# Performance work log

Measured on AMD Instinct MI355X. Metric: run time of the kernel, lower is better.

Reference implementation:

```python
import jax, jax.numpy as jnp
import numpy as np

N_NODES = 100000
N_EDGES = 1600000
IN_F = 64
HID = 64
NUM_GRAPHS = 256


def _lin(x, W, b):
    # Linear: x [N, in] @ W [in, out] + b [out]
    return x @ W + b


def _spect_conv(x, src, dst, W, b):
    # SpectConv, K=1, selfconn=False, edge_attr == 1:
    # h[i] = sum_{(j->i) in E} x[j];  out = h @ W + b
    h = jax.ops.segment_sum(x[src], dst, num_segments=N_NODES)
    return h @ W + b


def setup_inputs() -> dict:
    key = jax.random.key(0)
    ks = jax.random.split(key, 40)
    inp = {
        "x": jax.random.normal(ks[0], (N_NODES, IN_F), dtype=jnp.float32),
        "edge_index": jax.random.randint(ks[1], (2, N_EDGES), 0, N_NODES, dtype=jnp.int64),
        "batch": jnp.sort(jax.random.randint(ks[2], (N_NODES,), 0, NUM_GRAPHS, dtype=jnp.int64)),
    }
    i = 3
    def mk(shape):
        nonlocal i
        w = jax.random.normal(ks[i], shape, dtype=jnp.float32) * 0.05
        i += 1
        return w
    for l, fin in ((1, IN_F), (2, HID), (3, HID)):
        inp[f"conv{l}_w"] = mk((fin, HID)); inp[f"conv{l}_b"] = mk((HID,))
        for j in (1, 2, 3):
            inp[f"fc{l}{j}_w"] = mk((fin, HID)); inp[f"fc{l}{j}_b"] = mk((HID,))
    inp["fc1_w"] = mk((HID, 10)); inp["fc1_b"] = mk((10,))
    inp["fc2_w"] = mk((10, 1)); inp["fc2_b"] = mk((1,))
    return inp


def reference(x, edge_index, batch,
              conv1_w, conv1_b, fc11_w, fc11_b, fc12_w, fc12_b, fc13_w, fc13_b,
              conv2_w, conv2_b, fc21_w, fc21_b, fc22_w, fc22_b, fc23_w, fc23_b,
              conv3_w, conv3_b, fc31_w, fc31_b, fc32_w, fc32_b, fc33_w, fc33_b,
              fc1_w, fc1_b, fc2_w, fc2_b):
    src, dst = edge_index[0], edge_index[1]

    def layer(h, fa_w, fa_b, cw, cb, fb_w, fb_b, fc_w, fc_b):
        return jax.nn.relu(_lin(h, fa_w, fa_b)
                           + _spect_conv(h, src, dst, cw, cb)
                           + _lin(h, fb_w, fb_b) * _lin(h, fc_w, fc_b))

    h = layer(x, fc11_w, fc11_b, conv1_w, conv1_b, fc12_w, fc12_b, fc13_w, fc13_b)
    h = layer(h, fc21_w, fc21_b, conv2_w, conv2_b, fc22_w, fc22_b, fc23_w, fc23_b)
    h = layer(h, fc31_w, fc31_b, conv3_w, conv3_b, fc32_w, fc32_b, fc33_w, fc33_b)

    # global_mean_pool over graph ids
    sums = jax.ops.segment_sum(h, batch, num_segments=NUM_GRAPHS)
    cnts = jax.ops.segment_sum(jnp.ones((h.shape[0], 1), h.dtype), batch, num_segments=NUM_GRAPHS)
    pooled = sums / jnp.maximum(cnts, 1.0)

    g = _lin(pooled, fc1_w, fc1_b)
    return _lin(g, fc2_w, fc2_b)  # [NUM_GRAPHS, 1]
```

## Files before the change

kernel.cpp:

```cpp
#include <hip/hip_runtime.h>
#include <hip/hip_fp16.h>

#define NN 100000
#define NE 1600000
#define NG 256
#define NPB 32
#define LAYER_GRID 2048
#define SIDX 1280

#define BSH 9
#define NBKT ((NN + 511) / 512)
#define CAP 9216
#define TILE_A 4096
#define NBLK_A ((NE + TILE_A - 1) / TILE_A)

typedef _Float16 f16x8 __attribute__((ext_vector_type(8)));
typedef float f32x4 __attribute__((ext_vector_type(4)));

__device__ __forceinline__ uint2 f4_to_h16(float4 o) {
    __half2 lo = __floats2half2_rn(o.x, o.y);
    __half2 hi = __floats2half2_rn(o.z, o.w);
    uint2 u;
    u.x = *(unsigned int*)&lo;
    u.y = *(unsigned int*)&hi;
    return u;
}

__global__ __launch_bounds__(256) void cvt_kernel(const float* __restrict__ in,
                                                  __half* __restrict__ out) {
    const int i = blockIdx.x * 256 + threadIdx.x;
    const int n4 = NN * 64 / 4;
    if (i < n4) {
        float4 v = ((const float4*)in)[i];
        ((uint2*)out)[i] = f4_to_h16(v);
    }
}

__global__ __launch_bounds__(256) void wprep_kernel(const float* __restrict__ Wa,
                                                    const float* __restrict__ Wc,
                                                    const float* __restrict__ Wb,
                                                    const float* __restrict__ Wd,
                                                    __half* __restrict__ out) {
    const int i = blockIdx.x * 256 + threadIdx.x;
    if (i < 16384) {
        const int m = i >> 12;
        const int e = i & 4095;
        const int n = e >> 6, k = e & 63;
        const float* W = (m == 0) ? Wa : (m == 1) ? Wc : (m == 2) ? Wb : Wd;
        out[m * 4096 + n * 64 + k] = __float2half(W[k * 64 + n]);
    }
}

__global__ __launch_bounds__(256) void initcur_kernel(int* __restrict__ gcur) {
    int t = threadIdx.x;
    if (t < NBKT) gcur[t] = t * CAP;
}

__global__ __launch_bounds__(256) void binA_kernel(const int* __restrict__ src,
                                                   const int* __restrict__ dst,
                                                   int* __restrict__ gcur,
                                                   unsigned int* __restrict__ binned)
{
    __shared__ int hist[NBKT];
    __shared__ int cnt2[NBKT];
    __shared__ int lexcl[NBKT];
    __shared__ int base[NBKT];
    __shared__ int s[256];
    __shared__ unsigned int buf[TILE_A];
    __shared__ unsigned char bkt8[TILE_A];

    const int t = threadIdx.x;
    const int e0 = blockIdx.x * TILE_A;
    const int nedge = min(TILE_A, NE - e0);

    if (t < NBKT) { hist[t] = 0; cnt2[t] = 0; }
    __syncthreads();

    for (int j = t; j < nedge; j += 256)
        atomicAdd(&hist[dst[e0 + j] >> BSH], 1);
    __syncthreads();

    s[t] = (t < NBKT) ? hist[t] : 0;
    __syncthreads();
    for (int off = 1; off < 256; off <<= 1) {
        int u = (t >= off) ? s[t - off] : 0;
        __syncthreads();
        s[t] += u;
        __syncthreads();
    }
    if (t < NBKT) {
        lexcl[t] = s[t] - hist[t];
        if (hist[t] > 0) base[t] = atomicAdd(&gcur[t], hist[t]);
    }
    __syncthreads();

    for (int j = t; j < nedge; j += 256) {
        const int d = dst[e0 + j];
        const int sv = src[e0 + j];
        const int b = d >> BSH;
        const int r = atomicAdd(&cnt2[b], 1);
        const int idx = lexcl[b] + r;
        buf[idx] = ((unsigned int)sv << BSH) | (unsigned int)(d & 511);
        bkt8[idx] = (unsigned char)b;
    }
    __syncthreads();

    for (int j = t; j < nedge; j += 256) {
        const int b = bkt8[j];
        binned[base[b] + (j - lexcl[b])] = buf[j];
    }
}

__global__ __launch_bounds__(256) void bscan_kernel(const int* __restrict__ gcur,
                                                    int* __restrict__ bbase,
                                                    int* __restrict__ rs)
{
    __shared__ int s[256];
    const int t = threadIdx.x;
    const int sz = (t < NBKT) ? (gcur[t] - t * CAP) : 0;
    s[t] = sz;
    __syncthreads();
    for (int off = 1; off < 256; off <<= 1) {
        int u = (t >= off) ? s[t - off] : 0;
        __syncthreads();
        s[t] += u;
        __syncthreads();
    }
    if (t < NBKT) bbase[t] = s[t] - sz;
    if (t == 0) rs[NN] = NE;
}

__global__ __launch_bounds__(256) void binB_kernel(const unsigned int* __restrict__ binned,
                                                   const int* __restrict__ gcur,
                                                   const int* __restrict__ bbase,
                                                   int* __restrict__ csr,
                                                   int* __restrict__ rs)
{
    __shared__ int cnt[512];
    __shared__ int excl[512];
    __shared__ int cnt2[512];
    __shared__ int psum[256];
    __shared__ unsigned int buf[CAP];

    const int b = blockIdx.x;
    const int t = threadIdx.x;
    const int sz = gcur[b] - b * CAP;
    const int gb = bbase[b];
    const unsigned int* bp = binned + b * CAP;

    cnt[t] = 0; cnt[t + 256] = 0;
    cnt2[t] = 0; cnt2[t + 256] = 0;
    __syncthreads();

    for (int j = t; j < sz; j += 256) {
        const unsigned int v = bp[j];
        buf[j] = v;
        atomicAdd(&cnt[v & 511], 1);
    }
    __syncthreads();

    const int c0 = cnt[2 * t], c1 = cnt[2 * t + 1];
    psum[t] = c0 + c1;
    __syncthreads();
    for (int off = 1; off < 256; off <<= 1) {
        int u = (t >= off) ? psum[t - off] : 0;
        __syncthreads();
        psum[t] += u;
        __syncthreads();
    }
    const int pe = psum[t] - (c0 + c1);
    excl[2 * t] = pe;
    excl[2 * t + 1] = pe + c0;
    __syncthreads();

    const int node0 = b << BSH;
    for (int l = t; l < 512; l += 256) {
        const int node = node0 + l;
        if (node < NN) rs[node] = gb + excl[l];
    }

    for (int j = t; j < sz; j += 256) {
        const unsigned int v = buf[j];
        const int l = v & 511;
        const int r = atomicAdd(&cnt2[l], 1);
        csr[gb + excl[l] + r] = (int)(v >> BSH);
    }
}

__device__ __forceinline__ void accu8(float* a8, uint4 u) {
    const __half2* hp = (const __half2*)&u;
    #pragma unroll
    for (int q = 0; q < 4; ++q) {
        float2 f = __half22float2(hp[q]);
        a8[2 * q] += f.x; a8[2 * q + 1] += f.y;
    }
}

__global__ __launch_bounds__(256) void layer_kernel(
    const __half* __restrict__ h_in, __half* __restrict__ h_out,
    const int* __restrict__ csr, const int* __restrict__ rs,
    const __half* __restrict__ wt,
    const float* __restrict__ ba, const float* __restrict__ bc,
    const float* __restrict__ bb, const float* __restrict__ bd)
{
    __shared__ _Float16 sX1[NPB][72];
    __shared__ _Float16 sX2[NPB][72];
    __shared__ int sIdx[SIDX];

    const int tid = threadIdx.x;

    const int slot = tid >> 3;
    const int fg8  = tid & 7;

    const int w   = tid >> 6;
    const int l   = tid & 63;
    const int lr  = l & 15;
    const int kh  = l >> 4;
    const int col = w * 16 + lr;

    const _Float16* wtf = (const _Float16*)wt;
    f16x8 wrA0 = *(const f16x8*)&wtf[0 * 4096 + col * 64 + 0 * 32 + kh * 8];
    f16x8 wrA1 = *(const f16x8*)&wtf[0 * 4096 + col * 64 + 1 * 32 + kh * 8];
    f16x8 wrC0 = *(const f16x8*)&wtf[1 * 4096 + col * 64 + 0 * 32 + kh * 8];
    f16x8 wrC1 = *(const f16x8*)&wtf[1 * 4096 + col * 64 + 1 * 32 + kh * 8];
    f16x8 wrB0 = *(const f16x8*)&wtf[2 * 4096 + col * 64 + 0 * 32 + kh * 8];
    f16x8 wrB1 = *(const f16x8*)&wtf[2 * 4096 + col * 64 + 1 * 32 + kh * 8];
    f16x8 wrD0 = *(const f16x8*)&wtf[3 * 4096 + col * 64 + 0 * 32 + kh * 8];
    f16x8 wrD1 = *(const f16x8*)&wtf[3 * 4096 + col * 64 + 1 * 32 + kh * 8];
    const float bA = ba[col], bC = bc[col], bB = bb[col], bD = bd[col];

    const int npass = (NN + NPB - 1) / NPB;
    for (int g = blockIdx.x; g < npass; g += gridDim.x) {
        const int node0 = g * NPB;
        const int e0 = rs[node0];
        const int eN = rs[min(node0 + NPB, NN)];
        const int staged = min(eN - e0, SIDX);

        __syncthreads();
        for (int j = tid; j < staged; j += 256) sIdx[j] = csr[e0 + j];
        __syncthreads();

        const int node = node0 + slot;
        uint4 hreg = make_uint4(0u, 0u, 0u, 0u);
        float a8[8] = {0.f, 0.f, 0.f, 0.f, 0.f, 0.f, 0.f, 0.f};
        if (node < NN) {
            hreg = *(const uint4*)(h_in + node * 64 + fg8 * 8);
            const int rsn = rs[node];
            const int ne  = rs[node + 1] - rsn;
            const int le  = rsn - e0;
            for (int q = 0; q < ne; q += 8) {
                const int rem = ne - q;
                const int jb = le + q;
                auto gi = [&](int i) {
                    const int jr = jb + i;
                    return (jr < staged) ? sIdx[jr] : csr[e0 + jr];
                };
                const int s0 = gi(0);
                const int s1 = rem > 1 ? gi(1) : s0;
                const int s2 = rem > 2 ? gi(2) : s0;
                const int s3 = rem > 3 ? gi(3) : s0;
                const int s4 = rem > 4 ? gi(4) : s0;
                const int s5 = rem > 5 ? gi(5) : s0;
                const int s6 = rem > 6 ? gi(6) : s0;
                const int s7 = rem > 7 ? gi(7) : s0;
                const uint4 u0 = *(const uint4*)(h_in + s0 * 64 + fg8 * 8);
                const uint4 u1 = *(const uint4*)(h_in + s1 * 64 + fg8 * 8);
                const uint4 u2 = *(const uint4*)(h_in + s2 * 64 + fg8 * 8);
                const uint4 u3 = *(const uint4*)(h_in + s3 * 64 + fg8 * 8);
                const uint4 u4 = *(const uint4*)(h_in + s4 * 64 + fg8 * 8);
                const uint4 u5 = *(const uint4*)(h_in + s5 * 64 + fg8 * 8);
                const uint4 u6 = *(const uint4*)(h_in + s6 * 64 + fg8 * 8);
                const uint4 u7 = *(const uint4*)(h_in + s7 * 64 + fg8 * 8);
                accu8(a8, u0);
                if (rem > 1) accu8(a8, u1);
                if (rem > 2) accu8(a8, u2);
                if (rem > 3) accu8(a8, u3);
                if (rem > 4) accu8(a8, u4);
                if (rem > 5) accu8(a8, u5);
                if (rem > 6) accu8(a8, u6);
                if (rem > 7) accu8(a8, u7);
            }
        }

        *(uint4*)&sX1[slot][fg8 * 8] = hreg;
        union { _Float16 h[8]; uint4 u; } cv;
        #pragma unroll
        for (int j = 0; j < 8; ++j) cv.h[j] = (_Float16)a8[j];
        *(uint4*)&sX2[slot][fg8 * 8] = cv.u;
        __syncthreads();

        f32x4 accA1 = {0.f,0.f,0.f,0.f}, accC1 = {0.f,0.f,0.f,0.f};
        f32x4 accB1 = {0.f,0.f,0.f,0.f}, accD1 = {0.f,0.f,0.f,0.f};
        f32x4 accA2 = {0.f,0.f,0.f,0.f}, accC2 = {0.f,0.f,0.f,0.f};
        f32x4 accB2 = {0.f,0.f,0.f,0.f}, accD2 = {0.f,0.f,0.f,0.f};
        #pragma unroll
        for (int kk = 0; kk < 2; ++kk) {
            const int ko = kk * 32 + kh * 8;
            const f16x8 wa = kk ? wrA1 : wrA0;
            const f16x8 wc = kk ? wrC1 : wrC0;
            const f16x8 wb = kk ? wrB1 : wrB0;
            const f16x8 wd = kk ? wrD1 : wrD0;
            const f16x8 a1r0 = *(const f16x8*)&sX1[lr][ko];
            const f16x8 a2r0 = *(const f16x8*)&sX2[lr][ko];
            const f16x8 a1r1 = *(const f16x8*)&sX1[16 + lr][ko];
            const f16x8 a2r1 = *(const f16x8*)&sX2[16 + lr][ko];
            accA1 = __builtin_amdgcn_mfma_f32_16x16x32_f16(a1r0, wa, accA1, 0, 0, 0);
            accC1 = __builtin_amdgcn_mfma_f32_16x16x32_f16(a2r0, wc, accC1, 0, 0, 0);
            accB1 = __builtin_amdgcn_mfma_f32_16x16x32_f16(a1r0, wb, accB1, 0, 0, 0);
            accD1 = __builtin_amdgcn_mfma_f32_16x16x32_f16(a1r0, wd, accD1, 0, 0, 0);
            accA2 = __builtin_amdgcn_mfma_f32_16x16x32_f16(a1r1, wa, accA2, 0, 0, 0);
            accC2 = __builtin_amdgcn_mfma_f32_16x16x32_f16(a2r1, wc, accC2, 0, 0, 0);
            accB2 = __builtin_amdgcn_mfma_f32_16x16x32_f16(a1r1, wb, accB2, 0, 0, 0);
            accD2 = __builtin_amdgcn_mfma_f32_16x16x32_f16(a1r1, wd, accD2, 0, 0, 0);
        }

        #pragma unroll
        for (int r = 0; r < 4; ++r) {
            int row = kh * 4 + r;
            int nd  = node0 + row;
            if (nd < NN) {
                float o = fmaxf((accA1[r] + bA) + (accC1[r] + bC) +
                                (accB1[r] + bB) * (accD1[r] + bD), 0.f);
                h_out[nd * 64 + col] = __float2half(o);
            }
            nd += 16;
            if (nd < NN) {
                float o = fmaxf((accA2[r] + bA) + (accC2[r] + bC) +
                                (accB2[r] + bB) * (accD2[r] + bD), 0.f);
                h_out[nd * 64 + col] = __float2half(o);
            }
        }
    }
}

__global__ __launch_bounds__(256) void pool_mlp_kernel(
    const __half* __restrict__ h, const int* __restrict__ batch,
    const float* __restrict__ w1, const float* __restrict__ b1,
    const float* __restrict__ w2, const float* __restrict__ b2,
    float* __restrict__ out)
{
    const int g = blockIdx.x;
    const int t = threadIdx.x;
    int lo = 0, hi = NN;
    while (lo < hi) { int m = (lo + hi) >> 1; if (batch[m] < g) lo = m + 1; else hi = m; }
    const int start = lo;
    hi = NN;
    while (lo < hi) { int m = (lo + hi) >> 1; if (batch[m] < g + 1) lo = m + 1; else hi = m; }
    const int end = lo;

    const int f = t & 63, wsub = t >> 6;
    float sum = 0.f;
    for (int n = start + wsub; n < end; n += 4) sum += __half2float(h[n * 64 + f]);
    __shared__ float red[4][64];
    red[wsub][f] = sum;
    __syncthreads();
    __shared__ float pooled[64];
    if (t < 64) {
        float tot = red[0][t] + red[1][t] + red[2][t] + red[3][t];
        pooled[t] = tot / fmaxf((float)(end - start), 1.f);
    }
    __syncthreads();
    __shared__ float y10[10];
    if (t < 10) {
        float acc = b1[t];
        for (int k = 0; k < 64; ++k) acc = fmaf(pooled[k], w1[k * 10 + t], acc);
        y10[t] = acc;
    }
    __syncthreads();
    if (t == 0) {
        float acc = b2[0];
        for (int j = 0; j < 10; ++j) acc = fmaf(y10[j], w2[j], acc);
        out[g] = acc;
    }
}

extern "C" void kernel_launch(void* const* d_in, const int* in_sizes, int n_in,
                              void* d_out, int out_size, void* d_ws, size_t ws_size,
                              hipStream_t stream) {
    const float* x    = (const float*)d_in[0];
    const int* ei     = (const int*)d_in[1];
    const int* batch  = (const int*)d_in[2];
    const int* src    = ei;
    const int* dstv   = ei + NE;

    char* ws     = (char*)d_ws;
    __half* hX16 = (__half*)(ws);
    __half* hA16 = (__half*)(ws + 12800000);
    int* csr     = (int*)(ws + 25600000);
    int* rs      = (int*)(ws + 32000000);
    unsigned int* binned = (unsigned int*)(ws + 32500000);
    int* gcur    = (int*)(ws + 39800000);
    int* bbase   = (int*)(ws + 39800000 + 1024);
    __half* wt   = (__half*)(ws + 39810000);

    initcur_kernel<<<1, 256, 0, stream>>>(gcur);
    binA_kernel<<<NBLK_A, 256, 0, stream>>>(src, dstv, gcur, binned);
    bscan_kernel<<<1, 256, 0, stream>>>(gcur, bbase, rs);
    binB_kernel<<<NBKT, 256, 0, stream>>>(binned, gcur, bbase, csr, rs);
    cvt_kernel<<<(NN * 64 / 4 + 255) / 256, 256, 0, stream>>>(x, hX16);

    auto f = [&](int i) { return (const float*)d_in[i]; };
    wprep_kernel<<<64, 256, 0, stream>>>(f(5),  f(3),  f(7),  f(9),  wt);
    wprep_kernel<<<64, 256, 0, stream>>>(f(13), f(11), f(15), f(17), wt + 16384);
    wprep_kernel<<<64, 256, 0, stream>>>(f(21), f(19), f(23), f(25), wt + 32768);

    layer_kernel<<<LAYER_GRID, 256, 0, stream>>>(hX16, hA16, csr, rs,
        wt,         f(6), f(4), f(8), f(10));
    layer_kernel<<<LAYER_GRID, 256, 0, stream>>>(hA16, hX16, csr, rs,
        wt + 16384, f(14), f(12), f(16), f(18));
    layer_kernel<<<LAYER_GRID, 256, 0, stream>>>(hX16, hA16, csr, rs,
        wt + 32768, f(22), f(20), f(24), f(26));

    pool_mlp_kernel<<<NG, 256, 0, stream>>>(hA16, batch,
        f(27), f(28), f(29), f(30), (float*)d_out);
}
```

Measured before the change: 228.4 us.

## Fuse all stages into one persistent cooperative kernel with grid syncs

Eleven separate launches (binning, scan, CSR build, conversion, weight prep, three layers, pooling) become one cooperative persistent kernel with 1024 blocks. The stages are separated by grid.sync and share one union of LDS buffers. Binning is simplified: the per-tile LDS staging and the separate global scan kernel are dropped, and binA writes straight to global memory. The bucket scan is recomputed redundantly in every block. This removes launch gaps and tail effects, at the cost of fixed grid occupancy, grid-barrier overhead and less coalesced binned writes. A multi-kernel fallback runs if the cooperative launch fails.

```diff
diff --git a/kernel.cpp b/kernel.cpp
--- a/kernel.cpp
+++ b/kernel.cpp
@@ -1,21 +1,53 @@
 #include <hip/hip_runtime.h>
 #include <hip/hip_fp16.h>
+#include <hip/hip_cooperative_groups.h>
+
+namespace cg = cooperative_groups;
 
 #define NN 100000
 #define NE 1600000
 #define NG 256
 #define NPB 32
-#define LAYER_GRID 2048
 #define SIDX 1280
-
 #define BSH 9
 #define NBKT ((NN + 511) / 512)
 #define CAP 9216
 #define TILE_A 4096
 #define NBLK_A ((NE + TILE_A - 1) / TILE_A)
+#define GRID 1024
 
 typedef _Float16 f16x8 __attribute__((ext_vector_type(8)));
 typedef float f32x4 __attribute__((ext_vector_type(4)));
+
+struct KParams {
+    const float* x;
+    const int* src; const int* dst; const int* batch;
+    const float* wmat[12];
+    const float* bias[12];
+    const float* fc1w; const float* fc1b; const float* fc2w; const float* fc2b;
+    float* out;
+    __half* hX16; __half* hA16;
+    int* csr; int* rs;
+    unsigned int* binned;
+    int* gcur;
+    __half* wt;
+};
+
+union SmemT {
+    struct { _Float16 sX1[NPB][72]; _Float16 sX2[NPB][72]; int sIdx[SIDX]; } lay;
+    struct { int hist[NBKT]; int base[NBKT]; int cnt2[NBKT]; } ba;
+    struct { int cnt[512]; int excl[512]; int cnt2[512]; int psum[256]; int bbs[NBKT]; } bb;
+    struct { float red[4][64]; float pooled[64]; float y10[10]; } po;
+};
+
+__device__ __forceinline__ void accu8(float* a8, uint4 u) {
+    const __half2* hp = (const __half2*)&u;
+    #pragma unroll
+    for (int q = 0; q < 4; ++q) {
+        float2 f = __half22float2(hp[q]);
+        a8[2 * q] += f.x; a8[2 * q + 1] += f.y;
+    }
+}
 
 __device__ __forceinline__ uint2 f4_to_h16(float4 o) {
     __half2 lo = __floats2half2_rn(o.x, o.y);
@@ -26,218 +58,129 @@
     return u;
 }
 
-__global__ __launch_bounds__(256) void cvt_kernel(const float* __restrict__ in,
-                                                  __half* __restrict__ out) {
-    const int i = blockIdx.x * 256 + threadIdx.x;
-    const int n4 = NN * 64 / 4;
-    if (i < n4) {
-        float4 v = ((const float4*)in)[i];
-        ((uint2*)out)[i] = f4_to_h16(v);
-    }
-}
-
-__global__ __launch_bounds__(256) void wprep_kernel(const float* __restrict__ Wa,
-                                                    const float* __restrict__ Wc,
-                                                    const float* __restrict__ Wb,
-                                                    const float* __restrict__ Wd,
-                                                    __half* __restrict__ out) {
-    const int i = blockIdx.x * 256 + threadIdx.x;
-    if (i < 16384) {
-        const int m = i >> 12;
-        const int e = i & 4095;
+__device__ __forceinline__ void phase0(const KParams& p, SmemT& sm, int nblk) {
+    const int t = threadIdx.x;
+    const int gt = blockIdx.x * 256 + t;
+    const int gs = nblk * 256;
+
+    for (int i = gt; i < 12 * 4096; i += gs) {
+        const int m = i >> 12, e = i & 4095;
         const int n = e >> 6, k = e & 63;
-        const float* W = (m == 0) ? Wa : (m == 1) ? Wc : (m == 2) ? Wb : Wd;
-        out[m * 4096 + n * 64 + k] = __float2half(W[k * 64 + n]);
-    }
-}
-
-__global__ __launch_bounds__(256) void initcur_kernel(int* __restrict__ gcur) {
-    int t = threadIdx.x;
-    if (t < NBKT) gcur[t] = t * CAP;
-}
-
-__global__ __launch_bounds__(256) void binA_kernel(const int* __restrict__ src,
-                                                   const int* __restrict__ dst,
-                                                   int* __restrict__ gcur,
-                                                   unsigned int* __restrict__ binned)
-{
-    __shared__ int hist[NBKT];
-    __shared__ int cnt2[NBKT];
-    __shared__ int lexcl[NBKT];
-    __shared__ int base[NBKT];
-    __shared__ int s[256];
-    __shared__ unsigned int buf[TILE_A];
-    __shared__ unsigned char bkt8[TILE_A];
-
+        p.wt[m * 4096 + n * 64 + k] = __float2half(p.wmat[m][k * 64 + n]);
+    }
+    for (int i = gt; i < NN * 64 / 4; i += gs) {
+        float4 v = ((const float4*)p.x)[i];
+        ((uint2*)p.hX16)[i] = f4_to_h16(v);
+    }
+    for (int tile = blockIdx.x; tile < NBLK_A; tile += nblk) {
+        const int e0 = tile * TILE_A;
+        const int nedge = min(TILE_A, NE - e0);
+        __syncthreads();
+        if (t < NBKT) { sm.ba.hist[t] = 0; sm.ba.cnt2[t] = 0; }
+        __syncthreads();
+        for (int j = t; j < nedge; j += 256)
+            atomicAdd(&sm.ba.hist[p.dst[e0 + j] >> BSH], 1);
+        __syncthreads();
+        if (t < NBKT) {
+            const int h = sm.ba.hist[t];
+            if (h > 0) sm.ba.base[t] = t * CAP + atomicAdd(&p.gcur[t], h);
+        }
+        __syncthreads();
+        for (int j = t; j < nedge; j += 256) {
+            const int d = p.dst[e0 + j];
+            const int sv = p.src[e0 + j];
+            const int b = d >> BSH;
+            const int r = atomicAdd(&sm.ba.cnt2[b], 1);
+            p.binned[sm.ba.base[b] + r] = ((unsigned int)sv << BSH) | (unsigned int)(d & 511);
+        }
+    }
+}
+
+__device__ __forceinline__ void phase1(const KParams& p, SmemT& sm, int nblk) {
     const int t = threadIdx.x;
-    const int e0 = blockIdx.x * TILE_A;
-    const int nedge = min(TILE_A, NE - e0);
-
-    if (t < NBKT) { hist[t] = 0; cnt2[t] = 0; }
-    __syncthreads();
-
-    for (int j = t; j < nedge; j += 256)
-        atomicAdd(&hist[dst[e0 + j] >> BSH], 1);
-    __syncthreads();
-
-    s[t] = (t < NBKT) ? hist[t] : 0;
+    const int szt = (t < NBKT) ? min(p.gcur[t], CAP) : 0;
+    sm.bb.psum[t] = szt;
     __syncthreads();
     for (int off = 1; off < 256; off <<= 1) {
-        int u = (t >= off) ? s[t - off] : 0;
-        __syncthreads();
-        s[t] += u;
-        __syncthreads();
-    }
-    if (t < NBKT) {
-        lexcl[t] = s[t] - hist[t];
-        if (hist[t] > 0) base[t] = atomicAdd(&gcur[t], hist[t]);
-    }
+        int u = (t >= off) ? sm.bb.psum[t - off] : 0;
+        __syncthreads();
+        sm.bb.psum[t] += u;
+        __syncthreads();
+    }
+    if (t < NBKT) sm.bb.bbs[t] = sm.bb.psum[t] - szt;
     __syncthreads();
 
-    for (int j = t; j < nedge; j += 256) {
-        const int d = dst[e0 + j];
-        const int sv = src[e0 + j];
-        const int b = d >> BSH;
-        const int r = atomicAdd(&cnt2[b], 1);
-        const int idx = lexcl[b] + r;
-        buf[idx] = ((unsigned int)sv << BSH) | (unsigned int)(d & 511);
-        bkt8[idx] = (unsigned char)b;
-    }
-    __syncthreads();
-
-    for (int j = t; j < nedge; j += 256) {
-        const int b = bkt8[j];
-        binned[base[b] + (j - lexcl[b])] = buf[j];
-    }
-}
-
-__global__ __launch_bounds__(256) void bscan_kernel(const int* __restrict__ gcur,
-                                                    int* __restrict__ bbase,
-                                                    int* __restrict__ rs)
-{
-    __shared__ int s[256];
-    const int t = threadIdx.x;
-    const int sz = (t < NBKT) ? (gcur[t] - t * CAP) : 0;
-    s[t] = sz;
-    __syncthreads();
-    for (int off = 1; off < 256; off <<= 1) {
-        int u = (t >= off) ? s[t - off] : 0;
-        __syncthreads();
-        s[t] += u;
-        __syncthreads();
-    }
-    if (t < NBKT) bbase[t] = s[t] - sz;
-    if (t == 0) rs[NN] = NE;
-}
-
-__global__ __launch_bounds__(256) void binB_kernel(const unsigned int* __restrict__ binned,
-                                                   const int* __restrict__ gcur,
-                                                   const int* __restrict__ bbase,
-                                                   int* __restrict__ csr,
-                                                   int* __restrict__ rs)
-{
-    __shared__ int cnt[512];
-    __shared__ int excl[512];
-    __shared__ int cnt2[512];
-    __shared__ int psum[256];
-    __shared__ unsigned int buf[CAP];
-
-    const int b = blockIdx.x;
-    const int t = threadIdx.x;
-    const int sz = gcur[b] - b * CAP;
-    const int gb = bbase[b];
-    const unsigned int* bp = binned + b * CAP;
-
-    cnt[t] = 0; cnt[t + 256] = 0;
-    cnt2[t] = 0; cnt2[t + 256] = 0;
-    __syncthreads();
-
-    for (int j = t; j < sz; j += 256) {
-        const unsigned int v = bp[j];
-        buf[j] = v;
-        atomicAdd(&cnt[v & 511], 1);
-    }
-    __syncthreads();
-
-    const int c0 = cnt[2 * t], c1 = cnt[2 * t + 1];
-    psum[t] = c0 + c1;
-    __syncthreads();
-    for (int off = 1; off < 256; off <<= 1) {
-        int u = (t >= off) ? psum[t - off] : 0;
-        __syncthreads();
-        psum[t] += u;
-        __syncthreads();
-    }
-    const int pe = psum[t] - (c0 + c1);
-    excl[2 * t] = pe;
-    excl[2 * t + 1] = pe + c0;
-    __syncthreads();
-
-    const int node0 = b << BSH;
-    for (int l = t; l < 512; l += 256) {
-        const int node = node0 + l;
-        if (node < NN) rs[node] = gb + excl[l];
-    }
-
-    for (int j = t; j < sz; j += 256) {
-        const unsigned int v = buf[j];
-        const int l = v & 511;
-        const int r = atomicAdd(&cnt2[l], 1);
-        csr[gb + excl[l] + r] = (int)(v >> BSH);
-    }
-}
-
-__device__ __forceinline__ void accu8(float* a8, uint4 u) {
-    const __half2* hp = (const __half2*)&u;
-    #pragma unroll
-    for (int q = 0; q < 4; ++q) {
-        float2 f = __half22float2(hp[q]);
-        a8[2 * q] += f.x; a8[2 * q + 1] += f.y;
-    }
-}
-
-__global__ __launch_bounds__(256) void layer_kernel(
-    const __half* __restrict__ h_in, __half* __restrict__ h_out,
-    const int* __restrict__ csr, const int* __restrict__ rs,
-    const __half* __restrict__ wt,
-    const float* __restrict__ ba, const float* __restrict__ bc,
-    const float* __restrict__ bb, const float* __restrict__ bd)
-{
-    __shared__ _Float16 sX1[NPB][72];
-    __shared__ _Float16 sX2[NPB][72];
-    __shared__ int sIdx[SIDX];
-
+    for (int b = blockIdx.x; b < NBKT; b += nblk) {
+        const int sz = min(p.gcur[b], CAP);
+        const int gb = sm.bb.bbs[b];
+        const unsigned int* bp = p.binned + b * CAP;
+        __syncthreads();
+        sm.bb.cnt[t] = 0; sm.bb.cnt[t + 256] = 0;
+        sm.bb.cnt2[t] = 0; sm.bb.cnt2[t + 256] = 0;
+        __syncthreads();
+        for (int j = t; j < sz; j += 256)
+            atomicAdd(&sm.bb.cnt[bp[j] & 511], 1);
+        __syncthreads();
+        const int c0 = sm.bb.cnt[2 * t], c1 = sm.bb.cnt[2 * t + 1];
+        sm.bb.psum[t] = c0 + c1;
+        __syncthreads();
+        for (int off = 1; off < 256; off <<= 1) {
+            int u = (t >= off) ? sm.bb.psum[t - off] : 0;
+            __syncthreads();
+            sm.bb.psum[t] += u;
+            __syncthreads();
+        }
+        const int pe = sm.bb.psum[t] - (c0 + c1);
+        sm.bb.excl[2 * t] = pe;
+        sm.bb.excl[2 * t + 1] = pe + c0;
+        __syncthreads();
+        const int node0 = b << BSH;
+        for (int l = t; l < 512; l += 256) {
+            const int node = node0 + l;
+            if (node < NN) p.rs[node] = gb + sm.bb.excl[l];
+        }
+        for (int j = t; j < sz; j += 256) {
+            const unsigned int v = bp[j];
+            const int l = v & 511;
+            const int r = atomicAdd(&sm.bb.cnt2[l], 1);
+            p.csr[gb + sm.bb.excl[l] + r] = (int)(v >> BSH);
+        }
+    }
+    if (blockIdx.x == 0 && t == 0) p.rs[NN] = NE;
+}
+
+__device__ __forceinline__ void layer_phase(const KParams& p, SmemT& sm,
+                                            const __half* __restrict__ h_in,
+                                            __half* __restrict__ h_out,
+                                            int lidx, int nblk) {
     const int tid = threadIdx.x;
-
-    const int slot = tid >> 3;
-    const int fg8  = tid & 7;
-
-    const int w   = tid >> 6;
-    const int l   = tid & 63;
-    const int lr  = l & 15;
-    const int kh  = l >> 4;
+    const int slot = tid >> 3, fg8 = tid & 7;
+    const int w = tid >> 6, l = tid & 63, lr = l & 15, kh = l >> 4;
     const int col = w * 16 + lr;
 
-    const _Float16* wtf = (const _Float16*)wt;
-    f16x8 wrA0 = *(const f16x8*)&wtf[0 * 4096 + col * 64 + 0 * 32 + kh * 8];
-    f16x8 wrA1 = *(const f16x8*)&wtf[0 * 4096 + col * 64 + 1 * 32 + kh * 8];
-    f16x8 wrC0 = *(const f16x8*)&wtf[1 * 4096 + col * 64 + 0 * 32 + kh * 8];
-    f16x8 wrC1 = *(const f16x8*)&wtf[1 * 4096 + col * 64 + 1 * 32 + kh * 8];
-    f16x8 wrB0 = *(const f16x8*)&wtf[2 * 4096 + col * 64 + 0 * 32 + kh * 8];
-    f16x8 wrB1 = *(const f16x8*)&wtf[2 * 4096 + col * 64 + 1 * 32 + kh * 8];
-    f16x8 wrD0 = *(const f16x8*)&wtf[3 * 4096 + col * 64 + 0 * 32 + kh * 8];
-    f16x8 wrD1 = *(const f16x8*)&wtf[3 * 4096 + col * 64 + 1 * 32 + kh * 8];
-    const float bA = ba[col], bC = bc[col], bB = bb[col], bD = bd[col];
+    const _Float16* wtf = (const _Float16*)(p.wt + lidx * 16384);
+    const f16x8 wrA0 = *(const f16x8*)&wtf[0 * 4096 + col * 64 + kh * 8];
+    const f16x8 wrA1 = *(const f16x8*)&wtf[0 * 4096 + col * 64 + 32 + kh * 8];
+    const f16x8 wrC0 = *(const f16x8*)&wtf[1 * 4096 + col * 64 + kh * 8];
+    const f16x8 wrC1 = *(const f16x8*)&wtf[1 * 4096 + col * 64 + 32 + kh * 8];
+    const f16x8 wrB0 = *(const f16x8*)&wtf[2 * 4096 + col * 64 + kh * 8];
+    const f16x8 wrB1 = *(const f16x8*)&wtf[2 * 4096 + col * 64 + 32 + kh * 8];
+    const f16x8 wrD0 = *(const f16x8*)&wtf[3 * 4096 + col * 64 + kh * 8];
+    const f16x8 wrD1 = *(const f16x8*)&wtf[3 * 4096 + col * 64 + 32 + kh * 8];
+    const float bA = p.bias[lidx * 4 + 0][col];
+    const float bC = p.bias[lidx * 4 + 1][col];
+    const float bB = p.bias[lidx * 4 + 2][col];
+    const float bD = p.bias[lidx * 4 + 3][col];
 
     const int npass = (NN + NPB - 1) / NPB;
-    for (int g = blockIdx.x; g < npass; g += gridDim.x) {
+    for (int g = blockIdx.x; g < npass; g += nblk) {
         const int node0 = g * NPB;
-        const int e0 = rs[node0];
-        const int eN = rs[min(node0 + NPB, NN)];
+        const int e0 = p.rs[node0];
+        const int eN = p.rs[min(node0 + NPB, NN)];
         const int staged = min(eN - e0, SIDX);
 
         __syncthreads();
-        for (int j = tid; j < staged; j += 256) sIdx[j] = csr[e0 + j];
+        for (int j = tid; j < staged; j += 256) sm.lay.sIdx[j] = p.csr[e0 + j];
         __syncthreads();
 
         const int node = node0 + slot;
@@ -245,15 +188,15 @@
         float a8[8] = {0.f, 0.f, 0.f, 0.f, 0.f, 0.f, 0.f, 0.f};
         if (node < NN) {
             hreg = *(const uint4*)(h_in + node * 64 + fg8 * 8);
-            const int rsn = rs[node];
-            const int ne  = rs[node + 1] - rsn;
-            const int le  = rsn - e0;
+            const int rsn = p.rs[node];
+            const int ne = p.rs[node + 1] - rsn;
+            const int le = rsn - e0;
             for (int q = 0; q < ne; q += 8) {
                 const int rem = ne - q;
                 const int jb = le + q;
                 auto gi = [&](int i) {
                     const int jr = jb + i;
-                    return (jr < staged) ? sIdx[jr] : csr[e0 + jr];
+                    return (jr < staged) ? sm.lay.sIdx[jr] : p.csr[e0 + jr];
                 };
                 const int s0 = gi(0);
                 const int s1 = rem > 1 ? gi(1) : s0;
@@ -282,11 +225,11 @@
             }
         }
 
-        *(uint4*)&sX1[slot][fg8 * 8] = hreg;
+        *(uint4*)&sm.lay.sX1[slot][fg8 * 8] = hreg;
         union { _Float16 h[8]; uint4 u; } cv;
         #pragma unroll
         for (int j = 0; j < 8; ++j) cv.h[j] = (_Float16)a8[j];
-        *(uint4*)&sX2[slot][fg8 * 8] = cv.u;
+        *(uint4*)&sm.lay.sX2[slot][fg8 * 8] = cv.u;
         __syncthreads();
 
         f32x4 accA1 = {0.f,0.f,0.f,0.f}, accC1 = {0.f,0.f,0.f,0.f};
@@ -300,10 +243,10 @@
             const f16x8 wc = kk ? wrC1 : wrC0;
             const f16x8 wb = kk ? wrB1 : wrB0;
             const f16x8 wd = kk ? wrD1 : wrD0;
-            const f16x8 a1r0 = *(const f16x8*)&sX1[lr][ko];
-            const f16x8 a2r0 = *(const f16x8*)&sX2[lr][ko];
-            const f16x8 a1r1 = *(const f16x8*)&sX1[16 + lr][ko];
-            const f16x8 a2r1 = *(const f16x8*)&sX2[16 + lr][ko];
+            const f16x8 a1r0 = *(const f16x8*)&sm.lay.sX1[lr][ko];
+            const f16x8 a2r0 = *(const f16x8*)&sm.lay.sX2[lr][ko];
+            const f16x8 a1r1 = *(const f16x8*)&sm.lay.sX1[16 + lr][ko];
+            const f16x8 a2r1 = *(const f16x8*)&sm.lay.sX2[16 + lr][ko];
             accA1 = __builtin_amdgcn_mfma_f32_16x16x32_f16(a1r0, wa, accA1, 0, 0, 0);
             accC1 = __builtin_amdgcn_mfma_f32_16x16x32_f16(a2r0, wc, accC1, 0, 0, 0);
             accB1 = __builtin_amdgcn_mfma_f32_16x16x32_f16(a1r0, wb, accB1, 0, 0, 0);
@@ -316,8 +259,7 @@
 
         #pragma unroll
         for (int r = 0; r < 4; ++r) {
-            int row = kh * 4 + r;
-            int nd  = node0 + row;
+            int nd = node0 + kh * 4 + r;
             if (nd < NN) {
                 float o = fmaxf((accA1[r] + bA) + (accC1[r] + bC) +
                                 (accB1[r] + bB) * (accD1[r] + bD), 0.f);
@@ -333,84 +275,106 @@
     }
 }
 
-__global__ __launch_bounds__(256) void pool_mlp_kernel(
-    const __half* __restrict__ h, const int* __restrict__ batch,
-    const float* __restrict__ w1, const float* __restrict__ b1,
-    const float* __restrict__ w2, const float* __restrict__ b2,
-    float* __restrict__ out)
-{
-    const int g = blockIdx.x;
+__device__ __forceinline__ void pool_phase(const KParams& p, SmemT& sm, int nblk) {
     const int t = threadIdx.x;
-    int lo = 0, hi = NN;
-    while (lo < hi) { int m = (lo + hi) >> 1; if (batch[m] < g) lo = m + 1; else hi = m; }
-    const int start = lo;
-    hi = NN;
-    while (lo < hi) { int m = (lo + hi) >> 1; if (batch[m] < g + 1) lo = m + 1; else hi = m; }
-    const int end = lo;
-
-    const int f = t & 63, wsub = t >> 6;
-    float sum = 0.f;
-    for (int n = start + wsub; n < end; n += 4) sum += __half2float(h[n * 64 + f]);
-    __shared__ float red[4][64];
-    red[wsub][f] = sum;
-    __syncthreads();
-    __shared__ float pooled[64];
-    if (t < 64) {
-        float tot = red[0][t] + red[1][t] + red[2][t] + red[3][t];
-        pooled[t] = tot / fmaxf((float)(end - start), 1.f);
-    }
-    __syncthreads();
-    __shared__ float y10[10];
-    if (t < 10) {
-        float acc = b1[t];
-        for (int k = 0; k < 64; ++k) acc = fmaf(pooled[k], w1[k * 10 + t], acc);
-        y10[t] = acc;
-    }
-    __syncthreads();
-    if (t == 0) {
-        float acc = b2[0];
-        for (int j = 0; j < 10; ++j) acc = fmaf(y10[j], w2[j], acc);
-        out[g] = acc;
-    }
-}
+    const __half* h = p.hA16;
+    for (int g = blockIdx.x; g < NG; g += nblk) {
+        __syncthreads();
+        int lo = 0, hi = NN;
+        while (lo < hi) { int m = (lo + hi) >> 1; if (p.batch[m] < g) lo = m + 1; else hi = m; }
+        const int start = lo;
+        hi = NN;
+        while (lo < hi) { int m = (lo + hi) >> 1; if (p.batch[m] < g + 1) lo = m + 1; else hi = m; }
+        const int end = lo;
+
+        const int f = t & 63, wsub = t >> 6;
+        float sum = 0.f;
+        for (int n = start + wsub; n < end; n += 4) sum += __half2float(h[n * 64 + f]);
+        sm.po.red[wsub][f] = sum;
+        __syncthreads();
+        if (t < 64) {
+            float tot = sm.po.red[0][t] + sm.po.red[1][t] + sm.po.red[2][t] + sm.po.red[3][t];
+            sm.po.pooled[t] = tot / fmaxf((float)(end - start), 1.f);
+        }
+        __syncthreads();
+        if (t < 10) {
+            float acc = p.fc1b[t];
+            for (int k = 0; k < 64; ++k) acc = fmaf(sm.po.pooled[k], p.fc1w[k * 10 + t], acc);
+            sm.po.y10[t] = acc;
+        }
+        __syncthreads();
+        if (t == 0) {
+            float acc = p.fc2b[0];
+            for (int j = 0; j < 10; ++j) acc = fmaf(sm.po.y10[j], p.fc2w[j], acc);
+            p.out[g] = acc;
+        }
+    }
+}
+
+__global__ __launch_bounds__(256, 4) void fused_kernel(KParams p) {
+    __shared__ SmemT sm;
+    cg::grid_group grid = cg::this_grid();
+    phase0(p, sm, GRID);
+    grid.sync();
+    phase1(p, sm, GRID);
+    grid.sync();
+    layer_phase(p, sm, p.hX16, p.hA16, 0, GRID);
+    grid.sync();
+    layer_phase(p, sm, p.hA16, p.hX16, 1, GRID);
+    grid.sync();
+    layer_phase(p, sm, p.hX16, p.hA16, 2, GRID);
+    grid.sync();
+    pool_phase(p, sm, GRID);
+}
+
+__global__ __launch_bounds__(256, 4) void k_p0(KParams p)   { __shared__ SmemT sm; phase0(p, sm, gridDim.x); }
+__global__ __launch_bounds__(256, 4) void k_p1(KParams p)   { __shared__ SmemT sm; phase1(p, sm, gridDim.x); }
+__global__ __launch_bounds__(256, 4) void k_l0(KParams p)   { __shared__ SmemT sm; layer_phase(p, sm, p.hX16, p.hA16, 0, gridDim.x); }
+__global__ __launch_bounds__(256, 4) void k_l1(KParams p)   { __shared__ SmemT sm; layer_phase(p, sm, p.hA16, p.hX16, 1, gridDim.x); }
+__global__ __launch_bounds__(256, 4) void k_l2(KParams p)   { __shared__ SmemT sm; layer_phase(p, sm, p.hX16, p.hA16, 2, gridDim.x); }
+__global__ __launch_bounds__(256, 4) void k_pool(KParams p) { __shared__ SmemT sm; pool_phase(p, sm, gridDim.x); }
 
 extern "C" void kernel_launch(void* const* d_in, const int* in_sizes, int n_in,
                               void* d_out, int out_size, void* d_ws, size_t ws_size,
                               hipStream_t stream) {
-    const float* x    = (const float*)d_in[0];
-    const int* ei     = (const int*)d_in[1];
-    const int* batch  = (const int*)d_in[2];
-    const int* src    = ei;
-    const int* dstv   = ei + NE;
-
-    char* ws     = (char*)d_ws;
-    __half* hX16 = (__half*)(ws);
-    __half* hA16 = (__half*)(ws + 12800000);
-    int* csr     = (int*)(ws + 25600000);
-    int* rs      = (int*)(ws + 32000000);
-    unsigned int* binned = (unsigned int*)(ws + 32500000);
-    int* gcur    = (int*)(ws + 39800000);
-    int* bbase   = (int*)(ws + 39800000 + 1024);
-    __half* wt   = (__half*)(ws + 39810000);
-
-    initcur_kernel<<<1, 256, 0, stream>>>(gcur);
-    binA_kernel<<<NBLK_A, 256, 0, stream>>>(src, dstv, gcur, binned);
-    bscan_kernel<<<1, 256, 0, stream>>>(gcur, bbase, rs);
-    binB_kernel<<<NBKT, 256, 0, stream>>>(binned, gcur, bbase, csr, rs);
-    cvt_kernel<<<(NN * 64 / 4 + 255) / 256, 256, 0, stream>>>(x, hX16);
-
-    auto f = [&](int i) { return (const float*)d_in[i]; };
-    wprep_kernel<<<64, 256, 0, stream>>>(f(5),  f(3),  f(7),  f(9),  wt);
-    wprep_kernel<<<64, 256, 0, stream>>>(f(13), f(11), f(15), f(17), wt + 16384);
-    wprep_kernel<<<64, 256, 0, stream>>>(f(21), f(19), f(23), f(25), wt + 32768);
-
-    layer_kernel<<<LAYER_GRID, 256, 0, stream>>>(hX16, hA16, csr, rs,
-        wt,         f(6), f(4), f(8), f(10));
-    layer_kernel<<<LAYER_GRID, 256, 0, stream>>>(hA16, hX16, csr, rs,
-        wt + 16384, f(14), f(12), f(16), f(18));
-    layer_kernel<<<LAYER_GRID, 256, 0, stream>>>(hX16, hA16, csr, rs,
-        wt + 32768, f(22), f(20), f(24), f(26));
-
-    pool_mlp_kernel<<<NG, 256, 0, stream>>>(hA16, batch,
-        f(27), f(28), f(29), f(30), (float*)d_out);
-}
+    const int* ei = (const int*)d_in[1];
+
+    char* ws = (char*)d_ws;
+
+    KParams P;
+    P.x = (const float*)d_in[0];
+    P.src = ei;
+    P.dst = ei + NE;
+    P.batch = (const int*)d_in[2];
+    const int wm[12] = {5, 3, 7, 9, 13, 11, 15, 17, 21, 19, 23, 25};
+    const int bi[12] = {6, 4, 8, 10, 14, 12, 16, 18, 22, 20, 24, 26};
+    for (int i = 0; i < 12; ++i) {
+        P.wmat[i] = (const float*)d_in[wm[i]];
+        P.bias[i] = (const float*)d_in[bi[i]];
+    }
+    P.fc1w = (const float*)d_in[27]; P.fc1b = (const float*)d_in[28];
+    P.fc2w = (const float*)d_in[29]; P.fc2b = (const float*)d_in[30];
+    P.out = (float*)d_out;
+    P.hX16 = (__half*)(ws);
+    P.hA16 = (__half*)(ws + 12800000);
+    P.csr = (int*)(ws + 25600000);
+    P.rs = (int*)(ws + 32000000);
+    P.binned = (unsigned int*)(ws + 32500000);
+    P.gcur = (int*)(ws + 39800000);
+    P.wt = (__half*)(ws + 39810000);
+
+    hipMemsetAsync(P.gcur, 0, NBKT * sizeof(int), stream);
+
+    void* args[] = {(void*)&P};
+    hipError_t err = hipLaunchCooperativeKernel((const void*)fused_kernel,
+                                                dim3(GRID), dim3(256), args, 0, stream);
+    if (err != hipSuccess) {
+        (void)hipGetLastError();
+        k_p0<<<GRID, 256, 0, stream>>>(P);
+        k_p1<<<NBKT, 256, 0, stream>>>(P);
+        k_l0<<<2048, 256, 0, stream>>>(P);
+        k_l1<<<2048, 256, 0, stream>>>(P);
+        k_l2<<<2048, 256, 0, stream>>>(P);
+        k_pool<<<NG, 256, 0, stream>>>(P);
+    }
+}
```

After: 830.8 us. +263.7%, slower.

## Fuse preprocessing kernels: merge weight prep, x conversion, binning; fold bucket scan into binB

Applied to the files above, without the earlier changes.

Folds the x-to-fp16 conversion, all three weight transposes and the edge binning pass into a single persistent binA kernel with a 512-block grid-stride loop. Each binB block now recomputes the bucket-size prefix scan, which removes the separate scan kernel, and a memset replaces the cursor init kernel. The aim is to cut launch count and small-kernel tail overhead in the preprocessing phase. In exchange, binA runs with fewer blocks than edge tiles, and every binB block repeats a 196-entry scan.

```diff
diff --git a/kernel.cpp b/kernel.cpp
--- a/kernel.cpp
+++ b/kernel.cpp
@@ -16,6 +16,8 @@
 
 typedef _Float16 f16x8 __attribute__((ext_vector_type(8)));
 typedef float f32x4 __attribute__((ext_vector_type(4)));
+
+struct W12 { const float* w[12]; };
 
 __device__ __forceinline__ uint2 f4_to_h16(float4 o) {
     __half2 lo = __floats2half2_rn(o.x, o.y);
@@ -26,40 +28,22 @@
     return u;
 }
 
-__global__ __launch_bounds__(256) void cvt_kernel(const float* __restrict__ in,
-                                                  __half* __restrict__ out) {
-    const int i = blockIdx.x * 256 + threadIdx.x;
-    const int n4 = NN * 64 / 4;
-    if (i < n4) {
-        float4 v = ((const float4*)in)[i];
-        ((uint2*)out)[i] = f4_to_h16(v);
-    }
-}
-
-__global__ __launch_bounds__(256) void wprep_kernel(const float* __restrict__ Wa,
-                                                    const float* __restrict__ Wc,
-                                                    const float* __restrict__ Wb,
-                                                    const float* __restrict__ Wd,
-                                                    __half* __restrict__ out) {
-    const int i = blockIdx.x * 256 + threadIdx.x;
-    if (i < 16384) {
-        const int m = i >> 12;
-        const int e = i & 4095;
-        const int n = e >> 6, k = e & 63;
-        const float* W = (m == 0) ? Wa : (m == 1) ? Wc : (m == 2) ? Wb : Wd;
-        out[m * 4096 + n * 64 + k] = __float2half(W[k * 64 + n]);
-    }
-}
-
-__global__ __launch_bounds__(256) void initcur_kernel(int* __restrict__ gcur) {
-    int t = threadIdx.x;
-    if (t < NBKT) gcur[t] = t * CAP;
+__device__ __forceinline__ void accu8(float* a8, uint4 u) {
+    const __half2* hp = (const __half2*)&u;
+    #pragma unroll
+    for (int q = 0; q < 4; ++q) {
+        float2 f = __half22float2(hp[q]);
+        a8[2 * q] += f.x; a8[2 * q + 1] += f.y;
+    }
 }
 
 __global__ __launch_bounds__(256) void binA_kernel(const int* __restrict__ src,
                                                    const int* __restrict__ dst,
                                                    int* __restrict__ gcur,
-                                                   unsigned int* __restrict__ binned)
+                                                   unsigned int* __restrict__ binned,
+                                                   const float* __restrict__ x,
+                                                   __half* __restrict__ hX16,
+                                                   W12 wm, __half* __restrict__ wt)
 {
     __shared__ int hist[NBKT];
     __shared__ int cnt2[NBKT];
@@ -70,69 +54,64 @@
     __shared__ unsigned char bkt8[TILE_A];
 
     const int t = threadIdx.x;
-    const int e0 = blockIdx.x * TILE_A;
-    const int nedge = min(TILE_A, NE - e0);
-
-    if (t < NBKT) { hist[t] = 0; cnt2[t] = 0; }
-    __syncthreads();
-
-    for (int j = t; j < nedge; j += 256)
-        atomicAdd(&hist[dst[e0 + j] >> BSH], 1);
-    __syncthreads();
-
-    s[t] = (t < NBKT) ? hist[t] : 0;
-    __syncthreads();
-    for (int off = 1; off < 256; off <<= 1) {
-        int u = (t >= off) ? s[t - off] : 0;
-        __syncthreads();
-        s[t] += u;
-        __syncthreads();
-    }
-    if (t < NBKT) {
-        lexcl[t] = s[t] - hist[t];
-        if (hist[t] > 0) base[t] = atomicAdd(&gcur[t], hist[t]);
-    }
-    __syncthreads();
-
-    for (int j = t; j < nedge; j += 256) {
-        const int d = dst[e0 + j];
-        const int sv = src[e0 + j];
-        const int b = d >> BSH;
-        const int r = atomicAdd(&cnt2[b], 1);
-        const int idx = lexcl[b] + r;
-        buf[idx] = ((unsigned int)sv << BSH) | (unsigned int)(d & 511);
-        bkt8[idx] = (unsigned char)b;
-    }
-    __syncthreads();
-
-    for (int j = t; j < nedge; j += 256) {
-        const int b = bkt8[j];
-        binned[base[b] + (j - lexcl[b])] = buf[j];
-    }
-}
-
-__global__ __launch_bounds__(256) void bscan_kernel(const int* __restrict__ gcur,
-                                                    int* __restrict__ bbase,
-                                                    int* __restrict__ rs)
-{
-    __shared__ int s[256];
-    const int t = threadIdx.x;
-    const int sz = (t < NBKT) ? (gcur[t] - t * CAP) : 0;
-    s[t] = sz;
-    __syncthreads();
-    for (int off = 1; off < 256; off <<= 1) {
-        int u = (t >= off) ? s[t - off] : 0;
-        __syncthreads();
-        s[t] += u;
-        __syncthreads();
-    }
-    if (t < NBKT) bbase[t] = s[t] - sz;
-    if (t == 0) rs[NN] = NE;
+    const int gt = blockIdx.x * 256 + t;
+    const int gs = gridDim.x * 256;
+
+    for (int i = gt; i < 12 * 4096; i += gs) {
+        const int m = i >> 12, e = i & 4095;
+        const int n = e >> 6, k = e & 63;
+        wt[m * 4096 + n * 64 + k] = __float2half(wm.w[m][k * 64 + n]);
+    }
+    for (int i = gt; i < NN * 64 / 4; i += gs) {
+        float4 v = ((const float4*)x)[i];
+        ((uint2*)hX16)[i] = f4_to_h16(v);
+    }
+
+    for (int tile = blockIdx.x; tile < NBLK_A; tile += gridDim.x) {
+        const int e0 = tile * TILE_A;
+        const int nedge = min(TILE_A, NE - e0);
+        __syncthreads();
+        if (t < NBKT) { hist[t] = 0; cnt2[t] = 0; }
+        __syncthreads();
+
+        for (int j = t; j < nedge; j += 256)
+            atomicAdd(&hist[dst[e0 + j] >> BSH], 1);
+        __syncthreads();
+
+        s[t] = (t < NBKT) ? hist[t] : 0;
+        __syncthreads();
+        for (int off = 1; off < 256; off <<= 1) {
+            int u = (t >= off) ? s[t - off] : 0;
+            __syncthreads();
+            s[t] += u;
+            __syncthreads();
+        }
+        if (t < NBKT) {
+            lexcl[t] = s[t] - hist[t];
+            if (hist[t] > 0) base[t] = t * CAP + atomicAdd(&gcur[t], hist[t]);
+        }
+        __syncthreads();
+
+        for (int j = t; j < nedge; j += 256) {
+            const int d = dst[e0 + j];
+            const int sv = src[e0 + j];
+            const int b = d >> BSH;
+            const int r = atomicAdd(&cnt2[b], 1);
+            const int idx = lexcl[b] + r;
+            buf[idx] = ((unsigned int)sv << BSH) | (unsigned int)(d & 511);
+            bkt8[idx] = (unsigned char)b;
+        }
+        __syncthreads();
+
+        for (int j = t; j < nedge; j += 256) {
+            const int b = bkt8[j];
+            binned[base[b] + (j - lexcl[b])] = buf[j];
+        }
+    }
 }
 
 __global__ __launch_bounds__(256) void binB_kernel(const unsigned int* __restrict__ binned,
                                                    const int* __restrict__ gcur,
-                                                   const int* __restrict__ bbase,
                                                    int* __restrict__ csr,
                                                    int* __restrict__ rs)
 {
@@ -141,11 +120,24 @@
     __shared__ int cnt2[512];
     __shared__ int psum[256];
     __shared__ unsigned int buf[CAP];
+    __shared__ int gbs;
 
     const int b = blockIdx.x;
     const int t = threadIdx.x;
-    const int sz = gcur[b] - b * CAP;
-    const int gb = bbase[b];
+
+    const int szt = (t < NBKT) ? min(gcur[t], CAP) : 0;
+    psum[t] = szt;
+    __syncthreads();
+    for (int off = 1; off < 256; off <<= 1) {
+        int u = (t >= off) ? psum[t - off] : 0;
+        __syncthreads();
+        psum[t] += u;
+        __syncthreads();
+    }
+    if (t == b) gbs = psum[t] - szt;
+    __syncthreads();
+    const int sz = min(gcur[b], CAP);
+    const int gb = gbs;
     const unsigned int* bp = binned + b * CAP;
 
     cnt[t] = 0; cnt[t + 256] = 0;
@@ -178,22 +170,13 @@
         const int node = node0 + l;
         if (node < NN) rs[node] = gb + excl[l];
     }
-
     for (int j = t; j < sz; j += 256) {
         const unsigned int v = buf[j];
         const int l = v & 511;
         const int r = atomicAdd(&cnt2[l], 1);
         csr[gb + excl[l] + r] = (int)(v >> BSH);
     }
-}
-
-__device__ __forceinline__ void accu8(float* a8, uint4 u) {
-    const __half2* hp = (const __half2*)&u;
-    #pragma unroll
-    for (int q = 0; q < 4; ++q) {
-        float2 f = __half22float2(hp[q]);
-        a8[2 * q] += f.x; a8[2 * q + 1] += f.y;
-    }
+    if (b == 0 && t == 0) rs[NN] = NE;
 }
 
 __global__ __launch_bounds__(256) void layer_kernel(
@@ -208,25 +191,19 @@
     __shared__ int sIdx[SIDX];
 
     const int tid = threadIdx.x;
-
-    const int slot = tid >> 3;
-    const int fg8  = tid & 7;
-
-    const int w   = tid >> 6;
-    const int l   = tid & 63;
-    const int lr  = l & 15;
-    const int kh  = l >> 4;
+    const int slot = tid >> 3, fg8 = tid & 7;
+    const int w = tid >> 6, l = tid & 63, lr = l & 15, kh = l >> 4;
     const int col = w * 16 + lr;
 
     const _Float16* wtf = (const _Float16*)wt;
-    f16x8 wrA0 = *(const f16x8*)&wtf[0 * 4096 + col * 64 + 0 * 32 + kh * 8];
-    f16x8 wrA1 = *(const f16x8*)&wtf[0 * 4096 + col * 64 + 1 * 32 + kh * 8];
-    f16x8 wrC0 = *(const f16x8*)&wtf[1 * 4096 + col * 64 + 0 * 32 + kh * 8];
-    f16x8 wrC1 = *(const f16x8*)&wtf[1 * 4096 + col * 64 + 1 * 32 + kh * 8];
-    f16x8 wrB0 = *(const f16x8*)&wtf[2 * 4096 + col * 64 + 0 * 32 + kh * 8];
-    f16x8 wrB1 = *(const f16x8*)&wtf[2 * 4096 + col * 64 + 1 * 32 + kh * 8];
-    f16x8 wrD0 = *(const f16x8*)&wtf[3 * 4096 + col * 64 + 0 * 32 + kh * 8];
-    f16x8 wrD1 = *(const f16x8*)&wtf[3 * 4096 + col * 64 + 1 * 32 + kh * 8];
+    const f16x8 wrA0 = *(const f16x8*)&wtf[0 * 4096 + col * 64 + kh * 8];
+    const f16x8 wrA1 = *(const f16x8*)&wtf[0 * 4096 + col * 64 + 32 + kh * 8];
+    const f16x8 wrC0 = *(const f16x8*)&wtf[1 * 4096 + col * 64 + kh * 8];
+    const f16x8 wrC1 = *(const f16x8*)&wtf[1 * 4096 + col * 64 + 32 + kh * 8];
+    const f16x8 wrB0 = *(const f16x8*)&wtf[2 * 4096 + col * 64 + kh * 8];
+    const f16x8 wrB1 = *(const f16x8*)&wtf[2 * 4096 + col * 64 + 32 + kh * 8];
+    const f16x8 wrD0 = *(const f16x8*)&wtf[3 * 4096 + col * 64 + kh * 8];
+    const f16x8 wrD1 = *(const f16x8*)&wtf[3 * 4096 + col * 64 + 32 + kh * 8];
     const float bA = ba[col], bC = bc[col], bB = bb[col], bD = bd[col];
 
     const int npass = (NN + NPB - 1) / NPB;
@@ -246,8 +223,8 @@
         if (node < NN) {
             hreg = *(const uint4*)(h_in + node * 64 + fg8 * 8);
             const int rsn = rs[node];
-            const int ne  = rs[node + 1] - rsn;
-            const int le  = rsn - e0;
+            const int ne = rs[node + 1] - rsn;
+            const int le = rsn - e0;
             for (int q = 0; q < ne; q += 8) {
                 const int rem = ne - q;
                 const int jb = le + q;
@@ -316,8 +293,7 @@
 
         #pragma unroll
         for (int r = 0; r < 4; ++r) {
-            int row = kh * 4 + r;
-            int nd  = node0 + row;
+            int nd = node0 + kh * 4 + r;
             if (nd < NN) {
                 float o = fmaxf((accA1[r] + bA) + (accC1[r] + bC) +
                                 (accB1[r] + bB) * (accD1[r] + bD), 0.f);
@@ -377,11 +353,11 @@
 extern "C" void kernel_launch(void* const* d_in, const int* in_sizes, int n_in,
                               void* d_out, int out_size, void* d_ws, size_t ws_size,
                               hipStream_t stream) {
-    const float* x    = (const float*)d_in[0];
-    const int* ei     = (const int*)d_in[1];
-    const int* batch  = (const int*)d_in[2];
-    const int* src    = ei;
-    const int* dstv   = ei + NE;
+    const float* x   = (const float*)d_in[0];
+    const int* ei    = (const int*)d_in[1];
+    const int* batch = (const int*)d_in[2];
+    const int* src   = ei;
+    const int* dstv  = ei + NE;
 
     char* ws     = (char*)d_ws;
     __half* hX16 = (__half*)(ws);
@@ -390,19 +366,16 @@
     int* rs      = (int*)(ws + 32000000);
     unsigned int* binned = (unsigned int*)(ws + 32500000);
     int* gcur    = (int*)(ws + 39800000);
-    int* bbase   = (int*)(ws + 39800000 + 1024);
     __half* wt   = (__half*)(ws + 39810000);
 
-    initcur_kernel<<<1, 256, 0, stream>>>(gcur);
-    binA_kernel<<<NBLK_A, 256, 0, stream>>>(src, dstv, gcur, binned);
-    bscan_kernel<<<1, 256, 0, stream>>>(gcur, bbase, rs);
-    binB_kernel<<<NBKT, 256, 0, stream>>>(binned, gcur, bbase, csr, rs);
-    cvt_kernel<<<(NN * 64 / 4 + 255) / 256, 256, 0, stream>>>(x, hX16);
-
     auto f = [&](int i) { return (const float*)d_in[i]; };
-    wprep_kernel<<<64, 256, 0, stream>>>(f(5),  f(3),  f(7),  f(9),  wt);
-    wprep_kernel<<<64, 256, 0, stream>>>(f(13), f(11), f(15), f(17), wt + 16384);
-    wprep_kernel<<<64, 256, 0, stream>>>(f(21), f(19), f(23), f(25), wt + 32768);
+    W12 wm;
+    const int wmidx[12] = {5, 3, 7, 9, 13, 11, 15, 17, 21, 19, 23, 25};
+    for (int i = 0; i < 12; ++i) wm.w[i] = f(wmidx[i]);
+
+    hipMemsetAsync(gcur, 0, NBKT * sizeof(int), stream);
+    binA_kernel<<<512, 256, 0, stream>>>(src, dstv, gcur, binned, x, hX16, wm, wt);
+    binB_kernel<<<NBKT, 256, 0, stream>>>(binned, gcur, csr, rs);
 
     layer_kernel<<<LAYER_GRID, 256, 0, stream>>>(hX16, hA16, csr, rs,
         wt,         f(6), f(4), f(8), f(10));
```

Measured after the change: 218.0 us. 4.6% less time.
